# Kernel tuning notes

Hardware: AMD Instinct MI355X
Metric: run time of the kernel (lower is better)

## Reference

```python
import jax, jax.numpy as jnp
import numpy as np
import math
from jax import lax

PATCHES = [(80, 15), (32, 6), (10, 5), (5, 3)]  # (width, height)
L = 8      # stack_num
C = 256    # channel


def leaky(x):
    return jnp.where(x >= 0, x, 0.2 * x)


def conv2d(x, w, b, stride=1, padding=0, dilation=1):
    # x: [N,C,H,W], w: [O,I,kh,kw]
    y = lax.conv_general_dilated(
        x, w, (stride, stride), [(padding, padding), (padding, padding)],
        rhs_dilation=(dilation, dilation),
        dimension_numbers=("NCHW", "OIHW", "NCHW"))
    return y + b[None, :, None, None]


def upsample2_bilinear_ac(x):
    # F.interpolate(scale_factor=2, mode='bilinear', align_corners=True)
    N, Cc, H, W = x.shape
    def grid(n_in, n_out):
        c = jnp.arange(n_out, dtype=jnp.float32) * (n_in - 1) / (n_out - 1)
        i0 = jnp.floor(c).astype(jnp.int32)
        i1 = jnp.minimum(i0 + 1, n_in - 1)
        return i0, i1, c - i0.astype(jnp.float32)
    y0, y1, wy = grid(H, 2 * H)
    x0, x1, wx = grid(W, 2 * W)
    rows = x[:, :, y0, :] * (1.0 - wy)[None, None, :, None] + x[:, :, y1, :] * wy[None, None, :, None]
    out = rows[:, :, :, x0] * (1.0 - wx)[None, None, None, :] + rows[:, :, :, x1] * wx[None, None, None, :]
    return out


def patch_attention(q, k, v, b, t, height, width):
    # q,k,v: [b*t, d_k, H, W]; global attention over all t*oh*ow windows
    bt, d_k, H, W = q.shape
    oh, ow = H // height, W // width
    D = d_k * height * width
    def to_tokens(z):
        z = z.reshape(b, t, d_k, oh, height, ow, width)
        return z.transpose(0, 1, 3, 5, 2, 4, 6).reshape(b, t * oh * ow, D)
    qt, kt, vt = to_tokens(q), to_tokens(k), to_tokens(v)
    scores = jnp.einsum('bnd,bmd->bnm', qt, kt) / math.sqrt(D)
    attn = jax.nn.softmax(scores, axis=-1)
    y = jnp.einsum('bnm,bmd->bnd', attn, vt)
    y = y.reshape(b, t, oh, ow, d_k, height, width)
    return y.transpose(0, 1, 4, 2, 5, 3, 6).reshape(bt, d_k, H, W)


def mha(x, b, qw, qb, kw, kb, vw, vb, ow_, ob):
    bt, c, H, W = x.shape
    t = bt // b
    d_k = c // len(PATCHES)
    q = conv2d(x, qw, qb)
    k = conv2d(x, kw, kb)
    v = conv2d(x, vw, vb)
    outs = []
    for i, (width, height) in enumerate(PATCHES):
        s = slice(i * d_k, (i + 1) * d_k)
        outs.append(patch_attention(q[:, s], k[:, s], v[:, s], b, t, height, width))
    out = jnp.concatenate(outs, axis=1)
    return leaky(conv2d(out, ow_, ob, padding=1))


def feed_forward(x, w1, b1, w2, b2):
    x = leaky(conv2d(x, w1, b1, padding=2, dilation=2))
    x = leaky(conv2d(x, w2, b2, padding=1))
    return x


def setup_inputs() -> dict:
    key = jax.random.key(0)
    ks = iter(jax.random.split(key, 40))
    def w(shape, s=0.02):
        return jax.random.normal(next(ks), shape, jnp.float32) * s
    inp = {"masked_frames": jax.random.normal(next(ks), (1, 16, 3, 120, 640), jnp.float32)}
    # encoder
    inp.update(enc_w0=w((64, 3, 3, 3)), enc_b0=jnp.zeros((64,)),
               enc_w1=w((64, 64, 3, 3)), enc_b1=jnp.zeros((64,)),
               enc_w2=w((128, 64, 3, 3)), enc_b2=jnp.zeros((128,)),
               enc_w3=w((C, 128, 3, 3)), enc_b3=jnp.zeros((C,)))
    # transformer blocks (stacked over L layers)
    inp.update(tq_w=w((L, C, C, 1, 1)), tq_b=jnp.zeros((L, C)),
               tk_w=w((L, C, C, 1, 1)), tk_b=jnp.zeros((L, C)),
               tv_w=w((L, C, C, 1, 1)), tv_b=jnp.zeros((L, C)),
               to_w=w((L, C, C, 3, 3)), to_b=jnp.zeros((L, C)),
               tf1_w=w((L, C, C, 3, 3)), tf1_b=jnp.zeros((L, C)),
               tf2_w=w((L, C, C, 3, 3)), tf2_b=jnp.zeros((L, C)))
    # decoder
    inp.update(d0_w=w((128, C, 3, 3)), d0_b=jnp.zeros((128,)),
               d1_w=w((64, 128, 3, 3)), d1_b=jnp.zeros((64,)),
               d2_w=w((64, 64, 3, 3)), d2_b=jnp.zeros((64,)),
               d3_w=w((3, 64, 3, 3)), d3_b=jnp.zeros((3,)))
    return inp


def reference(masked_frames, enc_w0, enc_b0, enc_w1, enc_b1, enc_w2, enc_b2,
              enc_w3, enc_b3, tq_w, tq_b, tk_w, tk_b, tv_w, tv_b, to_w, to_b,
              tf1_w, tf1_b, tf2_w, tf2_b, d0_w, d0_b, d1_w, d1_b, d2_w, d2_b,
              d3_w, d3_b):
    b, t, c, h, w_ = masked_frames.shape
    x = masked_frames.reshape(b * t, c, h, w_)
    # encoder
    x = leaky(conv2d(x, enc_w0, enc_b0, stride=2, padding=1))
    x = leaky(conv2d(x, enc_w1, enc_b1, stride=1, padding=1))
    x = leaky(conv2d(x, enc_w2, enc_b2, stride=2, padding=1))
    x = leaky(conv2d(x, enc_w3, enc_b3, stride=1, padding=1))
    # transformer stack
    for i in range(L):
        x = x + mha(x, b, tq_w[i], tq_b[i], tk_w[i], tk_b[i], tv_w[i], tv_b[i],
                    to_w[i], to_b[i])
        x = x + feed_forward(x, tf1_w[i], tf1_b[i], tf2_w[i], tf2_b[i])
    # decoder
    x = leaky(conv2d(upsample2_bilinear_ac(x), d0_w, d0_b, padding=1))
    x = leaky(conv2d(x, d1_w, d1_b, padding=1))
    x = leaky(conv2d(upsample2_bilinear_ac(x), d2_w, d2_b, padding=1))
    x = conv2d(x, d3_w, d3_b, padding=1)
    return jnp.tanh(x)
```

## Files before the change

kernel.cpp:

```cpp
#include <hip/hip_runtime.h>
#include <hip/hip_bf16.h>
#include <math.h>

#define ACT_NONE 0
#define ACT_LEAKY 1
#define ACT_TANH 2

typedef __attribute__((ext_vector_type(8))) short bf16x8;
typedef __attribute__((ext_vector_type(4))) float f32x4;
typedef unsigned short u16;

#define MFMA(a, b, c) __builtin_amdgcn_mfma_f32_16x16x32_bf16((bf16x8)(a), (bf16x8)(b), (c), 0, 0, 0)

static inline unsigned cdivu(long a, long b) { return (unsigned)((a + b - 1) / b); }

__device__ __forceinline__ u16 f2bf(float x) {
  union { __hip_bfloat16 h; u16 u; } cv;
  cv.h = __float2bfloat16(x);
  return cv.u;
}
__device__ __forceinline__ float bf2f(u16 b) {
  union { u16 u; __hip_bfloat16 h; } cv;
  cv.u = b;
  return __bfloat162float(cv.h);
}
__device__ __forceinline__ void splitw(float v, u16* ph, u16* pl) {
  u16 h = f2bf(v);
  *ph = h;
  *pl = f2bf(v - bf2f(h));
}
__device__ __forceinline__ void gload16(const void* g, void* l) {
  __builtin_amdgcn_global_load_lds(
      (const __attribute__((address_space(1))) unsigned int*)g,
      (__attribute__((address_space(3))) unsigned int*)l, 16, 0, 0);
}

template <int K, int S, int DIL>
__global__ __launch_bounds__(256) void conv2d_k(
    const float* __restrict__ x, const float* __restrict__ w,
    const float* __restrict__ bias, float* y, u16* clh, u16* cll, int WpO,
    int PoffO, long o_fstride, int N, int Cin, int Hin, int Win, int Cout,
    int Hout, int Wout, int pad, int act) {
  constexpr int TW = 8;
  constexpr int XL = (TW - 1) * S + (K - 1) * DIL + 1;
  int wq = (Wout + TW - 1) / TW;
  long gid = (long)blockIdx.x * 256 + threadIdx.x;
  long total = (long)N * Cout * Hout * wq;
  if (gid >= total) return;
  int xg = (int)(gid % wq);
  long r = gid / wq;
  int yo = (int)(r % Hout);
  r /= Hout;
  int oc = (int)(r % Cout);
  int n = (int)(r / Cout);

  float bv = bias[oc];
  float acc[TW];
#pragma unroll
  for (int j = 0; j < TW; ++j) acc[j] = bv;

  int xo0 = xg * TW;
  int xi0 = xo0 * S - pad;
  const float* xn = x + (long)n * Cin * Hin * Win;
  const float* wb = w + (long)oc * Cin * K * K;

  for (int ic = 0; ic < Cin; ++ic) {
    const float* xc = xn + (long)ic * Hin * Win;
    const float* wc = wb + ic * (K * K);
#pragma unroll
    for (int ky = 0; ky < K; ++ky) {
      int yi = yo * S - pad + ky * DIL;
      if ((unsigned)yi < (unsigned)Hin) {
        const float* row = xc + (long)yi * Win;
        float xr[XL];
#pragma unroll
        for (int i2 = 0; i2 < XL; ++i2) {
          int xi = xi0 + i2;
          xr[i2] = ((unsigned)xi < (unsigned)Win) ? row[xi] : 0.f;
        }
#pragma unroll
        for (int kx = 0; kx < K; ++kx) {
          float wv = wc[ky * K + kx];
#pragma unroll
          for (int j = 0; j < TW; ++j)
            acc[j] = fmaf(wv, xr[j * S + kx * DIL], acc[j]);
        }
      }
    }
  }

#pragma unroll
  for (int j = 0; j < TW; ++j) {
    if (xo0 + j < Wout) {
      float v = acc[j];
      if (act == ACT_LEAKY)
        v = v >= 0.f ? v : 0.2f * v;
      else if (act == ACT_TANH)
        v = tanhf(v);
      if (y) y[(((long)n * Cout + oc) * Hout + yo) * Wout + xo0 + j] = v;
      if (clh) {
        long off = (long)n * o_fstride +
                   ((long)(yo + PoffO) * WpO + (xo0 + j + PoffO)) * Cout + oc;
        splitw(v, &clh[off], &cll[off]);
      }
    }
  }
}

__global__ __launch_bounds__(256) void conv_enc0_cl(
    const float* __restrict__ x, const float* __restrict__ w,
    const float* __restrict__ bias, u16* __restrict__ clh,
    u16* __restrict__ cll) {
  __shared__ float ws[64][29];
  int t = threadIdx.x;
  for (int i = t; i < 64 * 27; i += 256) ws[i / 27][i % 27] = w[i];
  __syncthreads();
  int oc = t & 63;
  float bv = bias[oc];
  long s0 = (long)blockIdx.x * 32 + (t >> 6);
#pragma unroll
  for (int step = 0; step < 8; ++step) {
    long s = s0 + step * 4;
    int xo = (int)(s % 320);
    long r = s / 320;
    int yo = (int)(r % 60);
    int n = (int)(r / 60);
    float acc = bv;
    for (int ic = 0; ic < 3; ++ic) {
      const float* xp = x + ((long)n * 3 + ic) * 76800;
      const float* wp = ws[oc] + ic * 9;
#pragma unroll
      for (int ky = 0; ky < 3; ++ky) {
        int yi = yo * 2 - 1 + ky;
        if ((unsigned)yi < 120u) {
#pragma unroll
          for (int kx = 0; kx < 3; ++kx) {
            int xi = xo * 2 - 1 + kx;
            if ((unsigned)xi < 640u)
              acc = fmaf(wp[ky * 3 + kx], xp[yi * 640 + xi], acc);
          }
        }
      }
    }
    float v = acc >= 0.f ? acc : 0.2f * acc;
    long off = (long)n * 1327104 + ((long)(yo + 2) * 324 + (xo + 2)) * 64 + oc;
    splitw(v, &clh[off], &cll[off]);
  }
}

template <int WM, int WN>
__global__ __launch_bounds__(256) void conv_gemm_lds(
    const u16* __restrict__ Ah, const u16* __restrict__ Al,
    const u16* __restrict__ Bh, const u16* __restrict__ Bl,
    const float* __restrict__ bias, int Cin, int Cout, int Hout, int Wout,
    int Wp, int Poff, int S, int DIL, int pad, int taps, long a_fstride,
    int act, float* yout, long y_fstride, u16* Oh, u16* Ol, long o_fstride,
    int WpO, int PoffO, int useres) {
  constexpr int TM = WM * 64, TN = WN * 64;
  __shared__ u16 AsH[TM * 32], BsH[TN * 32], BsL[TN * 32];
  int t = threadIdx.x;
  int lane = t & 63;
  int w = t >> 6;
  int wr = w / WN, wc = w % WN;
  int l15 = lane & 15, l16 = lane >> 4;
  int HW = Hout * Wout;
  int row0 = blockIdx.x * TM;
  int col0 = blockIdx.y * TN;
  const u16* Afh = Ah + (long)blockIdx.z * a_fstride;

  int rs = t >> 2;
  int cs = (t & 3) * 8;
  long abase[WM];
#pragma unroll
  for (int c = 0; c < WM; ++c) {
    int s = row0 + rs + 64 * c;
    if (s >= HW) s = HW - 1;
    int yo = s / Wout, xo = s - yo * Wout;
    int yb = yo * S - pad + Poff, xb = xo * S - pad + Poff;
    abase[c] = ((long)yb * Wp + xb) * Cin + cs;
  }
  long bbase[WN];
#pragma unroll
  for (int c = 0; c < WN; ++c)
    bbase[c] = (long)(col0 + rs + 64 * c) * Cin + cs;
  int ldst = w * 512;

  f32x4 acc[4][4];
#pragma unroll
  for (int m = 0; m < 4; ++m)
#pragma unroll
    for (int n = 0; n < 4; ++n) acc[m][n] = (f32x4){0.f, 0.f, 0.f, 0.f};

  for (int tap = 0; tap < taps; ++tap) {
    int ky = tap / 3, kx = tap - ky * 3;
    long atap = ((long)ky * DIL * Wp + kx * DIL) * Cin;
    long btap = (long)tap * Cout * Cin;
    for (int ic0 = 0; ic0 < Cin; ic0 += 32) {
#pragma unroll
      for (int c = 0; c < WM; ++c)
        gload16(Afh + abase[c] + atap + ic0, AsH + c * 2048 + ldst);
#pragma unroll
      for (int c = 0; c < WN; ++c) {
        gload16(Bh + bbase[c] + btap + ic0, BsH + c * 2048 + ldst);
        gload16(Bl + bbase[c] + btap + ic0, BsL + c * 2048 + ldst);
      }
      __syncthreads();
      bf16x8 ah[4];
#pragma unroll
      for (int m = 0; m < 4; ++m) {
        int rrow = wr * 64 + m * 16 + l15;
        ah[m] = *(const bf16x8*)(AsH + rrow * 32 + l16 * 8);
      }
#pragma unroll
      for (int n = 0; n < 4; ++n) {
        int rcol = wc * 64 + n * 16 + l15;
        bf16x8 bh = *(const bf16x8*)(BsH + rcol * 32 + l16 * 8);
        bf16x8 bl = *(const bf16x8*)(BsL + rcol * 32 + l16 * 8);
#pragma unroll
        for (int m = 0; m < 4; ++m) {
          acc[m][n] = MFMA(ah[m], bh, acc[m][n]);
          acc[m][n] = MFMA(ah[m], bl, acc[m][n]);
        }
      }
      __syncthreads();
    }
  }

  float* yf = yout ? yout + (long)blockIdx.z * y_fstride : nullptr;
  u16* Ofh = Oh ? Oh + (long)blockIdx.z * o_fstride : nullptr;
  u16* Ofl = Ol ? Ol + (long)blockIdx.z * o_fstride : nullptr;
#pragma unroll
  for (int m = 0; m < 4; ++m) {
#pragma unroll
    for (int r = 0; r < 4; ++r) {
      int s = row0 + wr * 64 + m * 16 + l16 * 4 + r;
      if (s >= HW) continue;
      int yo = s / Wout, xo = s - yo * Wout;
      long clbase = 0;
      if (Ofh) clbase = ((long)(yo + PoffO) * WpO + (xo + PoffO)) * Cout;
#pragma unroll
      for (int n = 0; n < 4; ++n) {
        int oc = col0 + wc * 64 + n * 16 + l15;
        float v = acc[m][n][r] + bias[oc];
        if (act == ACT_LEAKY) v = v >= 0.f ? v : 0.2f * v;
        if (Ofh) {
          long off = clbase + oc;
          if (useres) v += bf2f(Ofh[off]) + bf2f(Ofl[off]);
          splitw(v, &Ofh[off], &Ofl[off]);
        }
        if (yf) yf[((long)oc * Hout + yo) * Wout + xo] = v;
      }
    }
  }
}

__global__ __launch_bounds__(256) void qkv3_gemm_lds(
    const u16* __restrict__ Ah, const u16* __restrict__ Al, long a_fstride,
    int Wp, int Poff, const u16* __restrict__ qwh, const u16* __restrict__ qwl,
    const u16* __restrict__ kwh, const u16* __restrict__ kwl,
    const u16* __restrict__ vwh, const u16* __restrict__ vwl,
    const float* __restrict__ qbias, const float* __restrict__ kbias,
    const float* __restrict__ vbias, const int* __restrict__ nmap,
    const int* __restrict__ dmap, int ohow, int Dd, int pp, int NtokPad,
    float scale, u16* __restrict__ tqh, u16* __restrict__ tql,
    u16* __restrict__ tkh, u16* __restrict__ tkl, u16* __restrict__ tvh,
    u16* __restrict__ tvl) {
  __shared__ u16 AsH[256 * 32], BsH[64 * 32], BsL[64 * 32];
  int t = threadIdx.x;
  int lane = t & 63;
  int w = t >> 6;
  int l15 = lane & 15, l16 = lane >> 4;
  int row0 = blockIdx.x * 256;
  int frame = blockIdx.z;
  const u16* Afh = Ah + (long)frame * a_fstride;

  int rs = t >> 2;
  int cs = (t & 3) * 8;
  long abase[4];
#pragma unroll
  for (int c = 0; c < 4; ++c) {
    int s = row0 + rs + 64 * c;
    if (s >= 4800) s = 4799;
    int yo = s / 160, xo = s - yo * 160;
    abase[c] = ((long)(yo + Poff) * Wp + (xo + Poff)) * 256 + cs;
  }
  long bbase = (long)rs * 256 + cs;
  int ldst = w * 512;

  for (int mat = 0; mat < 3; ++mat) {
    const u16* Bh = mat == 0 ? qwh : mat == 1 ? kwh : vwh;
    const u16* Bl = mat == 0 ? qwl : mat == 1 ? kwl : vwl;
    const float* bias = mat == 0 ? qbias : mat == 1 ? kbias : vbias;
    u16* tH = mat == 0 ? tqh : mat == 1 ? tkh : tvh;
    u16* tL = mat == 0 ? tql : mat == 1 ? tkl : tvl;

    f32x4 acc[4][4];
#pragma unroll
    for (int m = 0; m < 4; ++m)
#pragma unroll
      for (int n = 0; n < 4; ++n) acc[m][n] = (f32x4){0.f, 0.f, 0.f, 0.f};

    for (int ic0 = 0; ic0 < 256; ic0 += 32) {
#pragma unroll
      for (int c = 0; c < 4; ++c)
        gload16(Afh + abase[c] + ic0, AsH + c * 2048 + ldst);
      gload16(Bh + bbase + ic0, BsH + ldst);
      gload16(Bl + bbase + ic0, BsL + ldst);
      __syncthreads();
      bf16x8 ah[4];
#pragma unroll
      for (int m = 0; m < 4; ++m) {
        int rrow = w * 64 + m * 16 + l15;
        ah[m] = *(const bf16x8*)(AsH + rrow * 32 + l16 * 8);
      }
#pragma unroll
      for (int n = 0; n < 4; ++n) {
        int rcol = n * 16 + l15;
        bf16x8 bh = *(const bf16x8*)(BsH + rcol * 32 + l16 * 8);
        bf16x8 bl = *(const bf16x8*)(BsL + rcol * 32 + l16 * 8);
#pragma unroll
        for (int m = 0; m < 4; ++m) {
          acc[m][n] = MFMA(ah[m], bh, acc[m][n]);
          acc[m][n] = MFMA(ah[m], bl, acc[m][n]);
        }
      }
      __syncthreads();
    }

#pragma unroll
    for (int m = 0; m < 4; ++m) {
#pragma unroll
      for (int r = 0; r < 4; ++r) {
        int s = row0 + w * 64 + m * 16 + l16 * 4 + r;
        if (s >= 4800) continue;
        int nm = nmap[s], dm = dmap[s];
        int ntok = frame * ohow + nm;
#pragma unroll
        for (int n = 0; n < 4; ++n) {
          int c = n * 16 + l15;
          float v = acc[m][n][r] + bias[c];
          if (mat == 0) v *= scale;
          int d = dm * 64 + c;
          long off = (mat == 2) ? ((long)d * NtokPad + ntok)
                                : ((long)ntok * Dd + d);
          u16 h = f2bf(v);
          tH[off] = h;
          if (mat != 0) tL[off] = f2bf(v - bf2f(h));
        }
      }
    }
  }
}

__global__ __launch_bounds__(256) void attn_gemm_lds(
    const u16* __restrict__ Ah, const u16* __restrict__ Al, int lda, int Mrows,
    const u16* __restrict__ Bh, const u16* __restrict__ Bl, int ldb,
    int Nclamp, int Kpart, int Nvalid, int mode, float* outf, int ldo,
    long partstride, u16* __restrict__ Oh, u16* __restrict__ Ol,
    const int* __restrict__ rowbase, const int* __restrict__ doff) {
  __shared__ u16 AsH[128 * 32], BsH[128 * 32], BsL[128 * 32];
  int t = threadIdx.x;
  int lane = t & 63;
  int w = t >> 6;
  int wc = w & 1, wr = w >> 1;
  int l15 = lane & 15, l16 = lane >> 4;
  int row0 = blockIdx.x * 128;
  int col0 = blockIdx.y * 128;
  int kbase = blockIdx.z * Kpart;
  if (outf) outf += (long)blockIdx.z * partstride;

  int rs = t >> 2;
  int cs = (t & 3) * 8;
  long abase[2], bbase[2];
#pragma unroll
  for (int c = 0; c < 2; ++c) {
    int sr = row0 + rs + 64 * c;
    if (sr >= Mrows) sr = Mrows - 1;
    abase[c] = (long)sr * lda + cs;
    int cc = col0 + rs + 64 * c;
    if (cc >= Nclamp) cc = Nclamp - 1;
    bbase[c] = (long)cc * ldb + cs;
  }
  int ldst = w * 512;

  f32x4 acc[4][4];
#pragma unroll
  for (int m = 0; m < 4; ++m)
#pragma unroll
    for (int n = 0; n < 4; ++n) acc[m][n] = (f32x4){0.f, 0.f, 0.f, 0.f};

  for (int k = kbase; k < kbase + Kpart; k += 32) {
#pragma unroll
    for (int c = 0; c < 2; ++c) {
      gload16(Ah + abase[c] + k, AsH + c * 2048 + ldst);
      gload16(Bh + bbase[c] + k, BsH + c * 2048 + ldst);
      gload16(Bl + bbase[c] + k, BsL + c * 2048 + ldst);
    }
    __syncthreads();
    bf16x8 ah[4];
#pragma unroll
    for (int m = 0; m < 4; ++m) {
      int rrow = wr * 64 + m * 16 + l15;
      ah[m] = *(const bf16x8*)(AsH + rrow * 32 + l16 * 8);
    }
#pragma unroll
    for (int n = 0; n < 4; ++n) {
      int rcol = wc * 64 + n * 16 + l15;
      bf16x8 bh = *(const bf16x8*)(BsH + rcol * 32 + l16 * 8);
      bf16x8 bl = *(const bf16x8*)(BsL + rcol * 32 + l16 * 8);
#pragma unroll
      for (int m = 0; m < 4; ++m) {
        acc[m][n] = MFMA(ah[m], bh, acc[m][n]);
        acc[m][n] = MFMA(ah[m], bl, acc[m][n]);
      }
    }
    __syncthreads();
  }

#pragma unroll
  for (int m = 0; m < 4; ++m) {
#pragma unroll
    for (int r = 0; r < 4; ++r) {
      int sr = row0 + wr * 64 + m * 16 + l16 * 4 + r;
      if (sr >= Mrows) continue;
#pragma unroll
      for (int n = 0; n < 4; ++n) {
        int c = col0 + wc * 64 + n * 16 + l15;
        if (c >= Nvalid) continue;
        float v = acc[m][n][r];
        if (mode == 0) {
          outf[(long)sr * ldo + c] = v;
        } else {
          long off = (long)rowbase[sr] + doff[c];
          splitw(v, &Oh[off], &Ol[off]);
        }
      }
    }
  }
}

__global__ __launch_bounds__(256) void attn_pv_lds(
    const float* __restrict__ P, int lda, int Mrows,
    const u16* __restrict__ Bh, const u16* __restrict__ Bl, int ldb,
    int Nclamp, int Kpart, int Nvalid, int mode, float* outf, int ldo,
    long partstride, u16* __restrict__ Oh, u16* __restrict__ Ol,
    const int* __restrict__ rowbase, const int* __restrict__ doff) {
  __shared__ float Asf[128 * 32];
  __shared__ u16 BsH[128 * 32], BsL[128 * 32];
  int t = threadIdx.x;
  int lane = t & 63;
  int w = t >> 6;
  int wc = w & 1, wr = w >> 1;
  int l15 = lane & 15, l16 = lane >> 4;
  int row0 = blockIdx.x * 128;
  int col0 = blockIdx.y * 128;
  int kbase = blockIdx.z * Kpart;
  if (outf) outf += (long)blockIdx.z * partstride;

  int arow = t >> 3;
  int acol = (t & 7) * 4;
  long abase[4];
#pragma unroll
  for (int j = 0; j < 4; ++j) {
    int r = row0 + arow + 32 * j;
    if (r >= Mrows) r = Mrows - 1;
    abase[j] = (long)r * lda + acol;
  }
  int rs = t >> 2;
  int cs = (t & 3) * 8;
  long bbase[2];
#pragma unroll
  for (int c = 0; c < 2; ++c) {
    int cc = col0 + rs + 64 * c;
    if (cc >= Nclamp) cc = Nclamp - 1;
    bbase[c] = (long)cc * ldb + cs;
  }
  int ldst = w * 512;

  f32x4 acc[4][4];
#pragma unroll
  for (int m = 0; m < 4; ++m)
#pragma unroll
    for (int n = 0; n < 4; ++n) acc[m][n] = (f32x4){0.f, 0.f, 0.f, 0.f};

  for (int k = kbase; k < kbase + Kpart; k += 32) {
#pragma unroll
    for (int j = 0; j < 4; ++j)
      gload16(P + abase[j] + k, Asf + (w * 64 + 256 * j) * 4);
#pragma unroll
    for (int c = 0; c < 2; ++c) {
      gload16(Bh + bbase[c] + k, BsH + c * 2048 + ldst);
      gload16(Bl + bbase[c] + k, BsL + c * 2048 + ldst);
    }
    __syncthreads();
    bf16x8 ah[4];
#pragma unroll
    for (int m = 0; m < 4; ++m) {
      int rrow = wr * 64 + m * 16 + l15;
      const float* ap = Asf + rrow * 32 + l16 * 8;
      f32x4 p0 = *(const f32x4*)(ap);
      f32x4 p1 = *(const f32x4*)(ap + 4);
#pragma unroll
      for (int e = 0; e < 4; ++e) {
        ah[m][e] = (short)f2bf(p0[e]);
        ah[m][4 + e] = (short)f2bf(p1[e]);
      }
    }
#pragma unroll
    for (int n = 0; n < 4; ++n) {
      int rcol = wc * 64 + n * 16 + l15;
      bf16x8 bh = *(const bf16x8*)(BsH + rcol * 32 + l16 * 8);
      bf16x8 bl = *(const bf16x8*)(BsL + rcol * 32 + l16 * 8);
#pragma unroll
      for (int m = 0; m < 4; ++m) {
        acc[m][n] = MFMA(ah[m], bh, acc[m][n]);
        acc[m][n] = MFMA(ah[m], bl, acc[m][n]);
      }
    }
    __syncthreads();
  }

#pragma unroll
  for (int m = 0; m < 4; ++m) {
#pragma unroll
    for (int r = 0; r < 4; ++r) {
      int sr = row0 + wr * 64 + m * 16 + l16 * 4 + r;
      if (sr >= Mrows) continue;
#pragma unroll
      for (int n = 0; n < 4; ++n) {
        int c = col0 + wc * 64 + n * 16 + l15;
        if (c >= Nvalid) continue;
        float v = acc[m][n][r];
        if (mode == 0) {
          outf[(long)sr * ldo + c] = v;
        } else {
          long off = (long)rowbase[sr] + doff[c];
          splitw(v, &Oh[off], &Ol[off]);
        }
      }
    }
  }
}

__global__ __launch_bounds__(256) void reduce_scatter(
    const float* __restrict__ parts, int nparts, long pstride, int rows, int N,
    int mode, float* outf, u16* __restrict__ Oh, u16* __restrict__ Ol,
    const int* __restrict__ rowbase, const int* __restrict__ doff) {
  long gid = (long)blockIdx.x * 256 + threadIdx.x;
  long tot = (long)rows * N;
  if (gid >= tot) return;
  float s = 0.f;
  for (int p = 0; p < nparts; ++p) s += parts[p * pstride + gid];
  if (mode == 0) {
    outf[gid] = s;
  } else {
    int r = (int)(gid / N), c = (int)(gid % N);
    long off = (long)rowbase[r] + doff[c];
    splitw(s, &Oh[off], &Ol[off]);
  }
}

__global__ __launch_bounds__(256) void softmax_ip(float* __restrict__ S,
                                                  int Ntok, int NtokPad) {
  int row = blockIdx.x;
  float* p = S + (long)row * NtokPad;
  __shared__ float red[256];
  int t = threadIdx.x;
  float m = -1e30f;
  for (int i = t; i < Ntok; i += 256) m = fmaxf(m, p[i]);
  red[t] = m;
  __syncthreads();
  for (int s = 128; s > 0; s >>= 1) {
    if (t < s) red[t] = fmaxf(red[t], red[t + s]);
    __syncthreads();
  }
  m = red[0];
  __syncthreads();
  float sum = 0.f;
  for (int i = t; i < Ntok; i += 256) sum += __expf(p[i] - m);
  red[t] = sum;
  __syncthreads();
  for (int s = 128; s > 0; s >>= 1) {
    if (t < s) red[t] += red[t + s];
    __syncthreads();
  }
  float inv = 1.f / red[0];
  __syncthreads();
  for (int i = t; i < Ntok; i += 256) p[i] = __expf(p[i] - m) * inv;
  for (int i = Ntok + t; i < NtokPad; i += 256) p[i] = 0.f;
}

__global__ __launch_bounds__(256) void wt_build(const float* __restrict__ w,
                                                int Cout, int Cin, int taps,
                                                u16* __restrict__ Wh,
                                                u16* __restrict__ Wl) {
  long gid = (long)blockIdx.x * 256 + threadIdx.x;
  long tot = (long)taps * Cout * Cin;
  if (gid >= tot) return;
  int ic = (int)(gid % Cin);
  long r = gid / Cin;
  int oc = (int)(r % Cout);
  int tap = (int)(r / Cout);
  float v = w[((long)oc * Cin + ic) * taps + tap];
  splitw(v, &Wh[gid], &Wl[gid]);
}

__global__ __launch_bounds__(256) void wt3_build(const float* __restrict__ w0,
                                                 const float* __restrict__ w1,
                                                 const float* __restrict__ w2,
                                                 u16* __restrict__ base) {
  long gid = (long)blockIdx.x * 256 + threadIdx.x;
  if (gid >= 3L * 589824) return;
  int mat = (int)(gid / 589824);
  int idx = (int)(gid - (long)mat * 589824);
  const float* w = mat == 0 ? w0 : mat == 1 ? w1 : w2;
  int ic = idx & 255;
  int r = idx >> 8;
  int oc = r & 255;
  int tap = r >> 8;
  float v = w[((long)oc * 256 + ic) * 9 + tap];
  u16* dst = base + (long)mat * 1179648;
  splitw(v, &dst[idx], &dst[589824 + idx]);
}

__global__ __launch_bounds__(256) void wtqkv_build_all(
    const float* __restrict__ wq, const float* __restrict__ wk,
    const float* __restrict__ wv, u16* __restrict__ qh, u16* __restrict__ ql,
    u16* __restrict__ kh, u16* __restrict__ kl, u16* __restrict__ vh,
    u16* __restrict__ vl) {
  int gid = blockIdx.x * 256 + threadIdx.x;
  if (gid >= 4 * 64 * 256) return;
  int ic = gid & 255;
  int c = (gid >> 8) & 63;
  int g = gid >> 14;
  long src = (long)(g * 64 + c) * 256 + ic;
  splitw(wq[src], &qh[gid], &ql[gid]);
  splitw(wk[src], &kh[gid], &kl[gid]);
  splitw(wv[src], &vh[gid], &vl[gid]);
}

__global__ __launch_bounds__(256) void maps_build(int ph, int pw, int ow,
                                                  int* __restrict__ nmap,
                                                  int* __restrict__ dmap) {
  int s = blockIdx.x * 256 + threadIdx.x;
  if (s >= 4800) return;
  int y = s / 160, x = s - y * 160;
  int i = y / ph, yy = y - i * ph;
  int j = x / pw, xx = x - j * pw;
  nmap[s] = i * ow + j;
  dmap[s] = yy * pw + xx;
}

__global__ __launch_bounds__(256) void luts_build(int ph, int pw, int ohow,
                                                  int ow, int pp, int Ntok,
                                                  int Dd, int gbase,
                                                  int* __restrict__ rowbase,
                                                  int* __restrict__ doff) {
  int gid = blockIdx.x * 256 + threadIdx.x;
  if (gid < Ntok) {
    int tt = gid / ohow, rem = gid - tt * ohow;
    int i = rem / ow, j = rem - i * ow;
    rowbase[gid] =
        tt * (32 * 162 * 256) + ((i * ph + 1) * 162 + (j * pw + 1)) * 256;
  }
  if (gid < Dd) {
    int ch = gid & 63;
    int dm = gid >> 6;
    int yy = dm / pw, xx = dm - yy * pw;
    doff[gid] = (yy * 162 + xx) * 256 + gbase + ch;
  }
}

__global__ __launch_bounds__(256) void up_cl2cl_pad(
    const u16* __restrict__ sh, const u16* __restrict__ sl,
    u16* __restrict__ oh, u16* __restrict__ ol, long s_fs, long o_fs, int C,
    int H, int W, int Wps, int Poffs, int Hp, int Wpo, int Poffo) {
  sh += (long)blockIdx.z * s_fs;
  sl += (long)blockIdx.z * s_fs;
  oh += (long)blockIdx.z * o_fs;
  ol += (long)blockIdx.z * o_fs;
  int Ho = 2 * H, Wo = 2 * W;
  long tot = (long)Hp * Wpo * C;
  long gid = (long)blockIdx.x * 256 + threadIdx.x;
  if (gid >= tot) return;
  int c = (int)(gid % C);
  long r = gid / C;
  int xp = (int)(r % Wpo);
  int yp = (int)(r / Wpo);
  int x = xp - Poffo, y = yp - Poffo;
  float v = 0.f;
  if ((unsigned)x < (unsigned)Wo && (unsigned)y < (unsigned)Ho) {
    float fy = (float)(y * (H - 1)) / (float)(Ho - 1);
    float fx = (float)(x * (W - 1)) / (float)(Wo - 1);
    int y0 = (int)fy, x0 = (int)fx;
    int y1 = min(y0 + 1, H - 1), x1 = min(x0 + 1, W - 1);
    float wy = fy - y0, wx = fx - x0;
    auto rd = [&](int cy, int cx) {
      long o = ((long)(cy + Poffs) * Wps + (cx + Poffs)) * C + c;
      return bf2f(sh[o]) + bf2f(sl[o]);
    };
    float r0 = rd(y0, x0) * (1.f - wx) + rd(y0, x1) * wx;
    float r1 = rd(y1, x0) * (1.f - wx) + rd(y1, x1) * wx;
    v = r0 * (1.f - wy) + r1 * wy;
  }
  splitw(v, &oh[gid], &ol[gid]);
}

extern "C" void kernel_launch(void* const* d_in, const int* in_sizes, int n_in,
                              void* d_out, int out_size, void* d_ws,
                              size_t ws_size, hipStream_t stream) {
  const float* input = (const float*)d_in[0];
  const float* enc_w0 = (const float*)d_in[1];
  const float* enc_b0 = (const float*)d_in[2];
  const float* enc_w1 = (const float*)d_in[3];
  const float* enc_b1 = (const float*)d_in[4];
  const float* enc_w2 = (const float*)d_in[5];
  const float* enc_b2 = (const float*)d_in[6];
  const float* enc_w3 = (const float*)d_in[7];
  const float* enc_b3 = (const float*)d_in[8];
  const float* tq_w = (const float*)d_in[9];
  const float* tq_b = (const float*)d_in[10];
  const float* tk_w = (const float*)d_in[11];
  const float* tk_b = (const float*)d_in[12];
  const float* tv_w = (const float*)d_in[13];
  const float* tv_b = (const float*)d_in[14];
  const float* to_w = (const float*)d_in[15];
  const float* to_b = (const float*)d_in[16];
  const float* tf1_w = (const float*)d_in[17];
  const float* tf1_b = (const float*)d_in[18];
  const float* tf2_w = (const float*)d_in[19];
  const float* tf2_b = (const float*)d_in[20];
  const float* d0_w = (const float*)d_in[21];
  const float* d0_b = (const float*)d_in[22];
  const float* d1_w = (const float*)d_in[23];
  const float* d1_b = (const float*)d_in[24];
  const float* d2_w = (const float*)d_in[25];
  const float* d2_b = (const float*)d_in[26];
  const float* d3_w = (const float*)d_in[27];
  const float* d3_b = (const float*)d_in[28];
  float* out = (float*)d_out;

  unsigned char* wsb = (unsigned char*)d_ws;
  size_t off = 0;
  auto alloc = [&](size_t bytes) {
    void* p = wsb + off;
    off = (off + bytes + 255) & ~(size_t)255;
    return p;
  };
  const long XCL_E = 22839296L;
  const long XCL2_E = 21233664L;
  const long QT_E = 4915200L;
  const long VT_E = 5111808L;
  u16* XCLh = (u16*)alloc(XCL_E * 2);
  u16* XCLl = (u16*)alloc(XCL_E * 2);
  u16* XCL2h = (u16*)alloc(XCL2_E * 2);
  u16* XCL2l = (u16*)alloc(XCL2_E * 2);
  u16* qth = (u16*)alloc(QT_E * 2);
  u16* qtl = (u16*)alloc(QT_E * 2);
  u16* kth = (u16*)alloc(QT_E * 2);
  u16* ktl = (u16*)alloc(QT_E * 2);
  u16* vth = (u16*)alloc(VT_E * 2);
  u16* vtl = (u16*)alloc(VT_E * 2);
  int* nmapA = (int*)alloc(4 * 4800 * 4);
  int* dmapA = (int*)alloc(4 * 4800 * 4);
  int* rowbaseA = (int*)alloc(7120 * 4);
  int* doffA = (int*)alloc(93248 * 4);
  u16* qwh = (u16*)alloc(65536 * 2);
  u16* qwl = (u16*)alloc(65536 * 2);
  u16* kwh = (u16*)alloc(65536 * 2);
  u16* kwl = (u16*)alloc(65536 * 2);
  u16* vwh = (u16*)alloc(65536 * 2);
  u16* vwl = (u16*)alloc(65536 * 2);
  size_t fixed_end = off;
  size_t avail = ws_size > fixed_end ? ws_size - fixed_end : 0;
  size_t SCB = avail > 4096 ? avail - 4096 : 0;
  if (SCB > 104857600UL) SCB = 104857600UL;
  float* scores = (float*)alloc(SCB);
  size_t need = off;
  if (ws_size < need) return;
  long SCAPf = (long)(SCB / 4);
  if (SCAPf < 1800000) return;

  u16* Wth = (u16*)scores;
  u16* Wtl = Wth + 589824;
  u16* W3 = (u16*)scores;

  unsigned char* decbase = (unsigned char*)XCL2h;
  u16* dec0inH = (u16*)(decbase + 0);
  u16* dec0inL = (u16*)(decbase + 40886272);
  u16* dec0outH = (u16*)(decbase + 81772544);
  u16* dec0outL = (u16*)(decbase + 102215680);
  u16* dec1outH = (u16*)(decbase + 122658816);
  u16* dec1outL = (u16*)(decbase + 132880384);
  u16* dec2inH = (u16*)(decbase + 0);
  u16* dec2inL = (u16*)(decbase + 20050944);
  float* dec2out = (float*)(decbase + 40101888);
  u16* Wd0h = (u16*)(decbase + 143101952);
  u16* Wd0l = Wd0h + 294912;
  u16* W1h = Wd0l + 294912;
  u16* W1l = W1h + 73728;
  u16* W2h = W1l + 73728;
  u16* W2l = W2h + 36864;
  const long D0IN_FS = 5110784, D0OUT_FS = 2555392, D1OUT_FS = 1277696;
  const long D2IN_FS = 5012736, D2OUT_FS = 4915200;

  const long FS_TR = 1427456;
  const long FS_T2 = 1327104;
  const long FS_E2 = 713728;

  static const int PWa[4] = {80, 32, 10, 5};
  static const int PHa[4] = {15, 6, 5, 3};
  static const int rbOff[4] = {0, 64, 464, 2000};
  static const int doOff[4] = {0, 76800, 89088, 92288};

  hipMemsetAsync(XCLh, 0, XCL_E * 2, stream);
  hipMemsetAsync(XCLl, 0, XCL_E * 2, stream);
  hipMemsetAsync(XCL2h, 0, XCL2_E * 2, stream);
  hipMemsetAsync(XCL2l, 0, XCL2_E * 2, stream);
  hipMemsetAsync(vth, 0, VT_E * 2, stream);
  hipMemsetAsync(vtl, 0, VT_E * 2, stream);
  conv_enc0_cl<<<9600, 256, 0, stream>>>(input, enc_w0, enc_b0, XCL2h, XCL2l);
  {
    wt_build<<<cdivu(9L * 64 * 64, 256), 256, 0, stream>>>(enc_w1, 64, 64, 9,
                                                           Wth, Wtl);
    conv_gemm_lds<4, 1><<<dim3(75, 1, 16), 256, 0, stream>>>(
        XCL2h, XCL2l, Wth, Wtl, enc_b1, 64, 64, 60, 320, 324, 2, 1, 1, 1, 9,
        FS_T2, ACT_LEAKY, nullptr, 0, XCLh, XCLl, FS_T2, 324, 2, 0);
  }
  hipMemsetAsync(XCL2h, 0, XCL2_E * 2, stream);
  hipMemsetAsync(XCL2l, 0, XCL2_E * 2, stream);
  {
    wt_build<<<cdivu(9L * 128 * 64, 256), 256, 0, stream>>>(enc_w2, 128, 64, 9,
                                                            Wth, Wtl);
    conv_gemm_lds<2, 2><<<dim3(38, 1, 16), 256, 0, stream>>>(
        XCLh, XCLl, Wth, Wtl, enc_b2, 64, 128, 30, 160, 324, 2, 2, 1, 1, 9,
        FS_T2, ACT_LEAKY, nullptr, 0, XCL2h, XCL2l, FS_E2, 164, 2, 0);
  }
  hipMemsetAsync(XCLh, 0, XCL_E * 2, stream);
  hipMemsetAsync(XCLl, 0, XCL_E * 2, stream);
  {
    wt_build<<<cdivu(9L * 256 * 128, 256), 256, 0, stream>>>(enc_w3, 256, 128,
                                                             9, Wth, Wtl);
    conv_gemm_lds<2, 2><<<dim3(38, 2, 16), 256, 0, stream>>>(
        XCL2h, XCL2l, Wth, Wtl, enc_b3, 128, 256, 30, 160, 164, 2, 1, 1, 1, 9,
        FS_E2, ACT_LEAKY, nullptr, 0, XCLh, XCLl, FS_TR, 164, 2, 0);
  }
  hipMemsetAsync(XCL2h, 0, XCL2_E * 2, stream);
  hipMemsetAsync(XCL2l, 0, XCL2_E * 2, stream);

  for (int g = 0; g < 4; ++g) {
    int ph = PHa[g], pw = PWa[g];
    int ohh = 30 / ph, oww = 160 / pw;
    int Ntok = 16 * ohh * oww, Dd = 64 * ph * pw, pp = ph * pw;
    maps_build<<<19, 256, 0, stream>>>(ph, pw, oww, nmapA + g * 4800,
                                       dmapA + g * 4800);
    int mx = Ntok > Dd ? Ntok : Dd;
    luts_build<<<cdivu(mx, 256), 256, 0, stream>>>(
        ph, pw, ohh * oww, oww, pp, Ntok, Dd, g * 64, rowbaseA + rbOff[g],
        doffA + doOff[g]);
  }

  for (int l = 0; l < 8; ++l) {
    wtqkv_build_all<<<256, 256, 0, stream>>>(
        tq_w + (long)l * 65536, tk_w + (long)l * 65536,
        tv_w + (long)l * 65536, qwh, qwl, kwh, kwl, vwh, vwl);

    for (int g = 0; g < 4; ++g) {
      int ph = PHa[g], pw = PWa[g];
      int ohh = 30 / ph, oww = 160 / pw;
      int ohow = ohh * oww;
      int Ntok = 16 * ohow, Dd = 64 * ph * pw, pp = ph * pw;
      int NtokPad = (Ntok + 31) & ~31;
      float scale = 1.0f / sqrtf((float)Dd);
      const int* nmap = nmapA + g * 4800;
      const int* dmap = dmapA + g * 4800;
      const int* rowbase = rowbaseA + rbOff[g];
      const int* doffp = doffA + doOff[g];

      qkv3_gemm_lds<<<dim3(19, 1, 16), 256, 0, stream>>>(
          XCLh, XCLl, FS_TR, 164, 2, qwh + g * 16384, qwl + g * 16384,
          kwh + g * 16384, kwl + g * 16384, vwh + g * 16384, vwl + g * 16384,
          tq_b + l * 256 + g * 64, tk_b + l * 256 + g * 64,
          tv_b + l * 256 + g * 64, nmap, dmap, ohow, Dd, pp, NtokPad, scale,
          qth, qtl, kth, ktl, vth, vtl);

      if (g == 0) {
        float* scoresR = scores + 131072;
        attn_gemm_lds<<<dim3(1, 1, 32), 256, 0, stream>>>(
            qth, qtl, Dd, 64, kth, ktl, Dd, 64, 2400, 64, 0, scores, 64, 4096,
            nullptr, nullptr, nullptr, nullptr);
        reduce_scatter<<<16, 256, 0, stream>>>(scores, 32, 4096, 64, 64, 0,
                                               scoresR, nullptr, nullptr,
                                               nullptr, nullptr);
        softmax_ip<<<64, 256, 0, stream>>>(scoresR, 64, 64);
        attn_pv_lds<<<dim3(1, 600, 1), 256, 0, stream>>>(
            scoresR, 64, 64, vth, vtl, 64, Dd, 64, Dd, 1, nullptr, 0, 0,
            XCL2h, XCL2l, rowbase, doffp);
      } else {
        long denom = (long)NtokPad + (g == 3 ? 3840 : 0);
        long cap = (SCAPf / denom) & ~127L;
        int chunk = (int)(cap < 128 ? 128 : cap);
        if (chunk > Ntok) chunk = Ntok;
        float* partials = scores + (long)chunk * NtokPad;
        for (int r0 = 0; r0 < Ntok; r0 += chunk) {
          int rows = Ntok - r0 < chunk ? Ntok - r0 : chunk;
          attn_gemm_lds<<<dim3(cdivu(rows, 128), cdivu(Ntok, 128), 1), 256, 0,
                          stream>>>(qth + (long)r0 * Dd, qtl + (long)r0 * Dd,
                                    Dd, rows, kth, ktl, Dd, Ntok, Dd, Ntok, 0,
                                    scores, NtokPad, 0, nullptr, nullptr,
                                    nullptr, nullptr);
          softmax_ip<<<rows, 256, 0, stream>>>(scores, Ntok, NtokPad);
          if (g == 3) {
            attn_pv_lds<<<dim3(cdivu(rows, 128), 8, 4), 256, 0, stream>>>(
                scores, NtokPad, rows, vth, vtl, NtokPad, Dd, 1280, Dd, 0,
                partials, 960, (long)rows * 960, nullptr, nullptr, nullptr,
                nullptr);
            reduce_scatter<<<cdivu((long)rows * 960, 256), 256, 0, stream>>>(
                partials, 4, (long)rows * 960, rows, 960, 1, nullptr, XCL2h,
                XCL2l, rowbase + r0, doffp);
          } else {
            attn_pv_lds<<<dim3(cdivu(rows, 128), Dd / 128, 1), 256, 0,
                          stream>>>(scores, NtokPad, rows, vth, vtl, NtokPad,
                                    Dd, NtokPad, Dd, 1, nullptr, 0, 0, XCL2h,
                                    XCL2l, rowbase + r0, doffp);
          }
        }
      }
    }

    wt3_build<<<6912, 256, 0, stream>>>(to_w + (long)l * 589824,
                                        tf1_w + (long)l * 589824,
                                        tf2_w + (long)l * 589824, W3);
    conv_gemm_lds<2, 2><<<dim3(38, 2, 16), 256, 0, stream>>>(
        XCL2h, XCL2l, W3, W3 + 589824, to_b + l * 256, 256, 256, 30, 160, 162,
        1, 1, 1, 1, 9, FS_T2, ACT_LEAKY, nullptr, 0, XCLh, XCLl, FS_TR, 164, 2,
        1);
    conv_gemm_lds<2, 2><<<dim3(38, 2, 16), 256, 0, stream>>>(
        XCLh, XCLl, W3 + 1179648, W3 + 1769472, tf1_b + l * 256, 256, 256, 30,
        160, 164, 2, 1, 2, 2, 9, FS_TR, ACT_LEAKY, nullptr, 0, XCL2h, XCL2l,
        FS_T2, 162, 1, 0);
    conv_gemm_lds<2, 2><<<dim3(38, 2, 16), 256, 0, stream>>>(
        XCL2h, XCL2l, W3 + 2359296, W3 + 2949120, tf2_b + l * 256, 256, 256,
        30, 160, 162, 1, 1, 1, 1, 9, FS_T2, ACT_LEAKY, nullptr, 0, XCLh, XCLl,
        FS_TR, 164, 2, 1);
  }

  hipMemsetAsync(decbase, 0, 144723968, stream);
  wt_build<<<cdivu(9L * 128 * 256, 256), 256, 0, stream>>>(d0_w, 128, 256, 9,
                                                           Wd0h, Wd0l);
  wt_build<<<cdivu(9L * 64 * 128, 256), 256, 0, stream>>>(d1_w, 64, 128, 9,
                                                          W1h, W1l);
  wt_build<<<cdivu(9L * 64 * 64, 256), 256, 0, stream>>>(d2_w, 64, 64, 9, W2h,
                                                         W2l);
  for (int f = 0; f < 16; f += 4) {
    up_cl2cl_pad<<<dim3(cdivu(62L * 322 * 256, 256), 1, 4), 256, 0, stream>>>(
        XCLh + (long)f * FS_TR, XCLl + (long)f * FS_TR, dec0inH, dec0inL,
        FS_TR, D0IN_FS, 256, 30, 160, 164, 2, 62, 322, 1);
    conv_gemm_lds<2, 2><<<dim3(150, 1, 4), 256, 0, stream>>>(
        dec0inH, dec0inL, Wd0h, Wd0l, d0_b, 256, 128, 60, 320, 322, 1, 1, 1, 1,
        9, D0IN_FS, ACT_LEAKY, nullptr, 0, dec0outH, dec0outL, D0OUT_FS, 322,
        1, 0);
    conv_gemm_lds<4, 1><<<dim3(75, 1, 4), 256, 0, stream>>>(
        dec0outH, dec0outL, W1h, W1l, d1_b, 128, 64, 60, 320, 322, 1, 1, 1, 1,
        9, D0OUT_FS, ACT_LEAKY, nullptr, 0, dec1outH, dec1outL, D1OUT_FS, 322,
        1, 0);
    for (int ff = 0; ff < 4; ff += 2) {
      up_cl2cl_pad<<<dim3(cdivu(122L * 642 * 64, 256), 1, 2), 256, 0,
                     stream>>>(dec1outH + (long)ff * D1OUT_FS,
                               dec1outL + (long)ff * D1OUT_FS, dec2inH,
                               dec2inL, D1OUT_FS, D2IN_FS, 64, 60, 320, 322, 1,
                               122, 642, 1);
      conv_gemm_lds<4, 1><<<dim3(300, 1, 2), 256, 0, stream>>>(
          dec2inH, dec2inL, W2h, W2l, d2_b, 64, 64, 120, 640, 642, 1, 1, 1, 1,
          9, D2IN_FS, ACT_LEAKY, dec2out, D2OUT_FS, nullptr, nullptr, 0, 0, 0,
          0);
      long tot = 2L * 3 * 120 * 80;
      conv2d_k<3, 1, 1><<<cdivu(tot, 256), 256, 0, stream>>>(
          dec2out, d3_w, d3_b, out + (long)(f + ff) * 230400, nullptr, nullptr,
          0, 0, 0, 2, 64, 120, 640, 3, 120, 640, 1, ACT_TANH);
    }
  }
}
```

Baseline: 27.67 ms.

## Double-buffer LDS tiles in conv, QKV and attention GEMM kernels

Converts the K loops of four LDS-tiled MFMA GEMM kernels into double-buffered pipelines. The next K-slice is staged into the alternate shared-memory buffer while the current one feeds the MFMAs, and one barrier per iteration is dropped. The aim is to hide global-to-LDS load latency behind compute. In exchange, LDS use per block doubles, which may lower occupancy. Correctness depends on gload16 semantics, since a direct-to-LDS async load would need suitable waits before the barrier.

```diff
diff --git a/kernel.cpp b/kernel.cpp
--- a/kernel.cpp
+++ b/kernel.cpp
@@ -157,7 +157,7 @@
     int act, float* yout, long y_fstride, u16* Oh, u16* Ol, long o_fstride,
     int WpO, int PoffO, int useres) {
   constexpr int TM = WM * 64, TN = WN * 64;
-  __shared__ u16 AsH[TM * 32], BsH[TN * 32], BsL[TN * 32];
+  __shared__ u16 AsH[2 * TM * 32], BsH[2 * TN * 32], BsL[2 * TN * 32];
   int t = threadIdx.x;
   int lane = t & 63;
   int w = t >> 6;
@@ -185,45 +185,60 @@
     bbase[c] = (long)(col0 + rs + 64 * c) * Cin + cs;
   int ldst = w * 512;
 
+  int nic = Cin >> 5;
+  int NK = taps * nic;
+  auto STAGE = [&](int kk, int buf) {
+    int tap = kk / nic;
+    int ic0 = (kk - tap * nic) << 5;
+    int ky = tap / 3, kx = tap - ky * 3;
+    long aoff = ((long)ky * DIL * Wp + kx * DIL) * Cin + ic0;
+    long boff = (long)tap * Cout * Cin + ic0;
+    u16* aB = AsH + buf * (TM * 32);
+    u16* bhB = BsH + buf * (TN * 32);
+    u16* blB = BsL + buf * (TN * 32);
+#pragma unroll
+    for (int c = 0; c < WM; ++c)
+      gload16(Afh + abase[c] + aoff, aB + c * 2048 + ldst);
+#pragma unroll
+    for (int c = 0; c < WN; ++c) {
+      gload16(Bh + bbase[c] + boff, bhB + c * 2048 + ldst);
+      gload16(Bl + bbase[c] + boff, blB + c * 2048 + ldst);
+    }
+  };
+
   f32x4 acc[4][4];
 #pragma unroll
   for (int m = 0; m < 4; ++m)
 #pragma unroll
     for (int n = 0; n < 4; ++n) acc[m][n] = (f32x4){0.f, 0.f, 0.f, 0.f};
 
-  for (int tap = 0; tap < taps; ++tap) {
-    int ky = tap / 3, kx = tap - ky * 3;
-    long atap = ((long)ky * DIL * Wp + kx * DIL) * Cin;
-    long btap = (long)tap * Cout * Cin;
-    for (int ic0 = 0; ic0 < Cin; ic0 += 32) {
-#pragma unroll
-      for (int c = 0; c < WM; ++c)
-        gload16(Afh + abase[c] + atap + ic0, AsH + c * 2048 + ldst);
-#pragma unroll
-      for (int c = 0; c < WN; ++c) {
-        gload16(Bh + bbase[c] + btap + ic0, BsH + c * 2048 + ldst);
-        gload16(Bl + bbase[c] + btap + ic0, BsL + c * 2048 + ldst);
-      }
-      __syncthreads();
-      bf16x8 ah[4];
+  STAGE(0, 0);
+  __syncthreads();
+  int cur = 0;
+  for (int kk = 0; kk < NK; ++kk) {
+    if (kk + 1 < NK) STAGE(kk + 1, cur ^ 1);
+    const u16* aB = AsH + cur * (TM * 32);
+    const u16* bhB = BsH + cur * (TN * 32);
+    const u16* blB = BsL + cur * (TN * 32);
+    bf16x8 ah[4];
+#pragma unroll
+    for (int m = 0; m < 4; ++m) {
+      int rrow = wr * 64 + m * 16 + l15;
+      ah[m] = *(const bf16x8*)(aB + rrow * 32 + l16 * 8);
+    }
+#pragma unroll
+    for (int n = 0; n < 4; ++n) {
+      int rcol = wc * 64 + n * 16 + l15;
+      bf16x8 bh = *(const bf16x8*)(bhB + rcol * 32 + l16 * 8);
+      bf16x8 bl = *(const bf16x8*)(blB + rcol * 32 + l16 * 8);
 #pragma unroll
       for (int m = 0; m < 4; ++m) {
-        int rrow = wr * 64 + m * 16 + l15;
-        ah[m] = *(const bf16x8*)(AsH + rrow * 32 + l16 * 8);
-      }
-#pragma unroll
-      for (int n = 0; n < 4; ++n) {
-        int rcol = wc * 64 + n * 16 + l15;
-        bf16x8 bh = *(const bf16x8*)(BsH + rcol * 32 + l16 * 8);
-        bf16x8 bl = *(const bf16x8*)(BsL + rcol * 32 + l16 * 8);
-#pragma unroll
-        for (int m = 0; m < 4; ++m) {
-          acc[m][n] = MFMA(ah[m], bh, acc[m][n]);
-          acc[m][n] = MFMA(ah[m], bl, acc[m][n]);
-        }
-      }
-      __syncthreads();
-    }
+        acc[m][n] = MFMA(ah[m], bh, acc[m][n]);
+        acc[m][n] = MFMA(ah[m], bl, acc[m][n]);
+      }
+    }
+    __syncthreads();
+    cur ^= 1;
   }
 
   float* yf = yout ? yout + (long)blockIdx.z * y_fstride : nullptr;
@@ -265,7 +280,7 @@
     float scale, u16* __restrict__ tqh, u16* __restrict__ tql,
     u16* __restrict__ tkh, u16* __restrict__ tkl, u16* __restrict__ tvh,
     u16* __restrict__ tvl) {
-  __shared__ u16 AsH[256 * 32], BsH[64 * 32], BsL[64 * 32];
+  __shared__ u16 AsH[2 * 256 * 32], BsH[2 * 64 * 32], BsL[2 * 64 * 32];
   int t = threadIdx.x;
   int lane = t & 63;
   int w = t >> 6;
@@ -294,30 +309,43 @@
     u16* tH = mat == 0 ? tqh : mat == 1 ? tkh : tvh;
     u16* tL = mat == 0 ? tql : mat == 1 ? tkl : tvl;
 
+    auto STAGE = [&](int kk, int buf) {
+      int ic0 = kk << 5;
+      u16* aB = AsH + buf * (256 * 32);
+      u16* bhB = BsH + buf * (64 * 32);
+      u16* blB = BsL + buf * (64 * 32);
+#pragma unroll
+      for (int c = 0; c < 4; ++c)
+        gload16(Afh + abase[c] + ic0, aB + c * 2048 + ldst);
+      gload16(Bh + bbase + ic0, bhB + ldst);
+      gload16(Bl + bbase + ic0, blB + ldst);
+    };
+
     f32x4 acc[4][4];
 #pragma unroll
     for (int m = 0; m < 4; ++m)
 #pragma unroll
       for (int n = 0; n < 4; ++n) acc[m][n] = (f32x4){0.f, 0.f, 0.f, 0.f};
 
-    for (int ic0 = 0; ic0 < 256; ic0 += 32) {
-#pragma unroll
-      for (int c = 0; c < 4; ++c)
-        gload16(Afh + abase[c] + ic0, AsH + c * 2048 + ldst);
-      gload16(Bh + bbase + ic0, BsH + ldst);
-      gload16(Bl + bbase + ic0, BsL + ldst);
-      __syncthreads();
+    STAGE(0, 0);
+    __syncthreads();
+    int cur = 0;
+    for (int kk = 0; kk < 8; ++kk) {
+      if (kk + 1 < 8) STAGE(kk + 1, cur ^ 1);
+      const u16* aB = AsH + cur * (256 * 32);
+      const u16* bhB = BsH + cur * (64 * 32);
+      const u16* blB = BsL + cur * (64 * 32);
       bf16x8 ah[4];
 #pragma unroll
       for (int m = 0; m < 4; ++m) {
         int rrow = w * 64 + m * 16 + l15;
-        ah[m] = *(const bf16x8*)(AsH + rrow * 32 + l16 * 8);
+        ah[m] = *(const bf16x8*)(aB + rrow * 32 + l16 * 8);
       }
 #pragma unroll
       for (int n = 0; n < 4; ++n) {
         int rcol = n * 16 + l15;
-        bf16x8 bh = *(const bf16x8*)(BsH + rcol * 32 + l16 * 8);
-        bf16x8 bl = *(const bf16x8*)(BsL + rcol * 32 + l16 * 8);
+        bf16x8 bh = *(const bf16x8*)(bhB + rcol * 32 + l16 * 8);
+        bf16x8 bl = *(const bf16x8*)(blB + rcol * 32 + l16 * 8);
 #pragma unroll
         for (int m = 0; m < 4; ++m) {
           acc[m][n] = MFMA(ah[m], bh, acc[m][n]);
@@ -325,6 +353,7 @@
         }
       }
       __syncthreads();
+      cur ^= 1;
     }
 
 #pragma unroll
@@ -358,7 +387,7 @@
     int Nclamp, int Kpart, int Nvalid, int mode, float* outf, int ldo,
     long partstride, u16* __restrict__ Oh, u16* __restrict__ Ol,
     const int* __restrict__ rowbase, const int* __restrict__ doff) {
-  __shared__ u16 AsH[128 * 32], BsH[128 * 32], BsL[128 * 32];
+  __shared__ u16 AsH[2 * 128 * 32], BsH[2 * 128 * 32], BsL[2 * 128 * 32];
   int t = threadIdx.x;
   int lane = t & 63;
   int w = t >> 6;
@@ -383,31 +412,45 @@
   }
   int ldst = w * 512;
 
+  int NK = Kpart >> 5;
+  auto STAGE = [&](int kk, int buf) {
+    long k = kbase + ((long)kk << 5);
+    u16* aB = AsH + buf * (128 * 32);
+    u16* bhB = BsH + buf * (128 * 32);
+    u16* blB = BsL + buf * (128 * 32);
+#pragma unroll
+    for (int c = 0; c < 2; ++c) {
+      gload16(Ah + abase[c] + k, aB + c * 2048 + ldst);
+      gload16(Bh + bbase[c] + k, bhB + c * 2048 + ldst);
+      gload16(Bl + bbase[c] + k, blB + c * 2048 + ldst);
+    }
+  };
+
   f32x4 acc[4][4];
 #pragma unroll
   for (int m = 0; m < 4; ++m)
 #pragma unroll
     for (int n = 0; n < 4; ++n) acc[m][n] = (f32x4){0.f, 0.f, 0.f, 0.f};
 
-  for (int k = kbase; k < kbase + Kpart; k += 32) {
-#pragma unroll
-    for (int c = 0; c < 2; ++c) {
-      gload16(Ah + abase[c] + k, AsH + c * 2048 + ldst);
-      gload16(Bh + bbase[c] + k, BsH + c * 2048 + ldst);
-      gload16(Bl + bbase[c] + k, BsL + c * 2048 + ldst);
-    }
-    __syncthreads();
+  STAGE(0, 0);
+  __syncthreads();
+  int cur = 0;
+  for (int kk = 0; kk < NK; ++kk) {
+    if (kk + 1 < NK) STAGE(kk + 1, cur ^ 1);
+    const u16* aB = AsH + cur * (128 * 32);
+    const u16* bhB = BsH + cur * (128 * 32);
+    const u16* blB = BsL + cur * (128 * 32);
     bf16x8 ah[4];
 #pragma unroll
     for (int m = 0; m < 4; ++m) {
       int rrow = wr * 64 + m * 16 + l15;
-      ah[m] = *(const bf16x8*)(AsH + rrow * 32 + l16 * 8);
+      ah[m] = *(const bf16x8*)(aB + rrow * 32 + l16 * 8);
     }
 #pragma unroll
     for (int n = 0; n < 4; ++n) {
       int rcol = wc * 64 + n * 16 + l15;
-      bf16x8 bh = *(const bf16x8*)(BsH + rcol * 32 + l16 * 8);
-      bf16x8 bl = *(const bf16x8*)(BsL + rcol * 32 + l16 * 8);
+      bf16x8 bh = *(const bf16x8*)(bhB + rcol * 32 + l16 * 8);
+      bf16x8 bl = *(const bf16x8*)(blB + rcol * 32 + l16 * 8);
 #pragma unroll
       for (int m = 0; m < 4; ++m) {
         acc[m][n] = MFMA(ah[m], bh, acc[m][n]);
@@ -415,6 +458,7 @@
       }
     }
     __syncthreads();
+    cur ^= 1;
   }
 
 #pragma unroll
@@ -445,8 +489,8 @@
     int Nclamp, int Kpart, int Nvalid, int mode, float* outf, int ldo,
     long partstride, u16* __restrict__ Oh, u16* __restrict__ Ol,
     const int* __restrict__ rowbase, const int* __restrict__ doff) {
-  __shared__ float Asf[128 * 32];
-  __shared__ u16 BsH[128 * 32], BsL[128 * 32];
+  __shared__ float Asf[2 * 128 * 32];
+  __shared__ u16 BsH[2 * 128 * 32], BsL[2 * 128 * 32];
   int t = threadIdx.x;
   int lane = t & 63;
   int w = t >> 6;
@@ -477,27 +521,41 @@
   }
   int ldst = w * 512;
 
+  int NK = Kpart >> 5;
+  auto STAGE = [&](int kk, int buf) {
+    long k = kbase + ((long)kk << 5);
+    float* aB = Asf + buf * (128 * 32);
+    u16* bhB = BsH + buf * (128 * 32);
+    u16* blB = BsL + buf * (128 * 32);
+#pragma unroll
+    for (int j = 0; j < 4; ++j)
+      gload16(P + abase[j] + k, aB + (w * 64 + 256 * j) * 4);
+#pragma unroll
+    for (int c = 0; c < 2; ++c) {
+      gload16(Bh + bbase[c] + k, bhB + c * 2048 + ldst);
+      gload16(Bl + bbase[c] + k, blB + c * 2048 + ldst);
+    }
+  };
+
   f32x4 acc[4][4];
 #pragma unroll
   for (int m = 0; m < 4; ++m)
 #pragma unroll
     for (int n = 0; n < 4; ++n) acc[m][n] = (f32x4){0.f, 0.f, 0.f, 0.f};
 
-  for (int k = kbase; k < kbase + Kpart; k += 32) {
-#pragma unroll
-    for (int j = 0; j < 4; ++j)
-      gload16(P + abase[j] + k, Asf + (w * 64 + 256 * j) * 4);
-#pragma unroll
-    for (int c = 0; c < 2; ++c) {
-      gload16(Bh + bbase[c] + k, BsH + c * 2048 + ldst);
-      gload16(Bl + bbase[c] + k, BsL + c * 2048 + ldst);
-    }
-    __syncthreads();
+  STAGE(0, 0);
+  __syncthreads();
+  int cur = 0;
+  for (int kk = 0; kk < NK; ++kk) {
+    if (kk + 1 < NK) STAGE(kk + 1, cur ^ 1);
+    const float* aB = Asf + cur * (128 * 32);
+    const u16* bhB = BsH + cur * (128 * 32);
+    const u16* blB = BsL + cur * (128 * 32);
     bf16x8 ah[4];
 #pragma unroll
     for (int m = 0; m < 4; ++m) {
       int rrow = wr * 64 + m * 16 + l15;
-      const float* ap = Asf + rrow * 32 + l16 * 8;
+      const float* ap = aB + rrow * 32 + l16 * 8;
       f32x4 p0 = *(const f32x4*)(ap);
       f32x4 p1 = *(const f32x4*)(ap + 4);
 #pragma unroll
@@ -509,8 +567,8 @@
 #pragma unroll
     for (int n = 0; n < 4; ++n) {
       int rcol = wc * 64 + n * 16 + l15;
-      bf16x8 bh = *(const bf16x8*)(BsH + rcol * 32 + l16 * 8);
-      bf16x8 bl = *(const bf16x8*)(BsL + rcol * 32 + l16 * 8);
+      bf16x8 bh = *(const bf16x8*)(bhB + rcol * 32 + l16 * 8);
+      bf16x8 bl = *(const bf16x8*)(blB + rcol * 32 + l16 * 8);
 #pragma unroll
       for (int m = 0; m < 4; ++m) {
         acc[m][n] = MFMA(ah[m], bh, acc[m][n]);
@@ -518,6 +576,7 @@
       }
     }
     __syncthreads();
+    cur ^= 1;
   }
 
 #pragma unroll
```

Result: faster. 26.59 ms (-3.9%).
